# Kernel optimization log

Hardware: AMD Instinct MI355X
Metric: run time of the kernel (lower is better)

The kernel has to match this reference:

```python
import jax, jax.numpy as jnp
import numpy as np

DIM = 512
HEADS = 8
DIM_HEAD = DIM // 8          # 64
INNER = HEADS * DIM_HEAD     # 512
M_LANDMARKS = DIM // 2       # 256
PINV_ITERS = 6
RES_KERNEL = 33
LN_EPS = 1e-5


def setup_inputs() -> dict:
    key = jax.random.key(0)
    ks = jax.random.split(key, 7)
    b, n = 8, 4096
    x = jax.random.normal(ks[0], (b, n, DIM), dtype=jnp.float32)
    gamma = jnp.ones((DIM,), jnp.float32)
    beta = jnp.zeros((DIM,), jnp.float32)
    w_qkv = jax.random.normal(ks[1], (DIM, 3 * INNER), jnp.float32) * 0.02
    w_out = jax.random.normal(ks[2], (INNER, DIM), jnp.float32) * 0.02
    b_out = jnp.zeros((DIM,), jnp.float32)
    # depthwise Conv2d(heads, heads, (33,1), groups=heads): torch weight [H,1,33,1]
    res_kernel = jax.random.normal(ks[3], (HEADS, 1, RES_KERNEL, 1), jnp.float32) * 0.05
    return {"x": x, "gamma": gamma, "beta": beta, "w_qkv": w_qkv,
            "w_out": w_out, "b_out": b_out, "res_kernel": res_kernel}


def _moore_penrose_pinv(a, iters=PINV_ITERS):
    # a: [b, h, m, m]
    abs_a = jnp.abs(a)
    col = abs_a.sum(axis=-1).max()   # global max, as in torch.max(col)
    row = abs_a.sum(axis=-2).max()
    z = jnp.swapaxes(a, -1, -2) / (col * row)
    I = jnp.eye(a.shape[-1], dtype=a.dtype)
    for _ in range(iters):
        az = a @ z
        z = 0.25 * z @ (13. * I - az @ (15. * I - az @ (7. * I - az)))
    return z


def _nystrom_attention(xn, w_qkv, res_kernel, w_out, b_out):
    b, n, _ = xn.shape
    h, dh, m = HEADS, DIM_HEAD, M_LANDMARKS
    scale = dh ** -0.5
    qkv = xn @ w_qkv                               # [b, n, 3*inner]
    q, k, v = jnp.split(qkv, 3, axis=-1)
    def to_heads(t):
        return t.reshape(b, n, h, dh).transpose(0, 2, 1, 3)  # [b,h,n,dh]
    q, k, v = to_heads(q), to_heads(k), to_heads(v)
    q = q * scale

    l = n // m  # n chosen as multiple of m -> no padding branch
    # landmark pooling: '(m l) d -> m d' mean
    q_l = q.reshape(b, h, m, l, dh).mean(axis=3)   # [b,h,m,dh]
    k_l = k.reshape(b, h, m, l, dh).mean(axis=3)

    sim1 = jnp.einsum('bhid,bhjd->bhij', q, k_l)    # [b,h,n,m]
    sim2 = jnp.einsum('bhid,bhjd->bhij', q_l, k_l)  # [b,h,m,m]
    sim3 = jnp.einsum('bhid,bhjd->bhij', q_l, k)    # [b,h,m,n]

    attn1 = jax.nn.softmax(sim1, axis=-1)
    attn2 = jax.nn.softmax(sim2, axis=-1)
    attn3 = jax.nn.softmax(sim3, axis=-1)

    attn2_inv = _moore_penrose_pinv(attn2)
    out = (attn1 @ attn2_inv) @ (attn3 @ v)         # [b,h,n,dh]

    # residual depthwise conv over sequence dim (kernel 33x1, groups=heads)
    pad = RES_KERNEL // 2
    out = out + jax.lax.conv_general_dilated(
        v, res_kernel, window_strides=(1, 1),
        padding=((pad, pad), (0, 0)),
        dimension_numbers=('NCHW', 'OIHW', 'NCHW'),
        feature_group_count=HEADS)

    out = out.transpose(0, 2, 1, 3).reshape(b, n, h * dh)  # [b,n,inner]
    return out @ w_out + b_out  # dropout omitted (eval mode)


def reference(x, gamma, beta, w_qkv, w_out, b_out, res_kernel):
    mu = x.mean(axis=-1, keepdims=True)
    var = x.var(axis=-1, keepdims=True)
    xn = (x - mu) * jax.lax.rsqrt(var + LN_EPS) * gamma + beta
    return x + _nystrom_attention(xn, w_qkv, res_kernel, w_out, b_out)
```

## Files before the change

### kernel.cpp

```cpp
#include <hip/hip_runtime.h>

#define SEQ 4096
#define DMODEL 512
#define NH 8
#define DH 64
#define MLM 256
#define NBH 64
#define NROWS 32768

typedef unsigned short bf16_t;
typedef __attribute__((ext_vector_type(8))) short bf16x8;
typedef __attribute__((ext_vector_type(4))) float f32x4;

__device__ __forceinline__ float bf2f(unsigned short u) {
  return __uint_as_float(((unsigned)u) << 16);
}
__device__ __forceinline__ unsigned short f2bf(float f) {
  unsigned u = __float_as_uint(f);
  u += 0x7fffu + ((u >> 16) & 1u);
  return (unsigned short)(u >> 16);
}
__device__ __forceinline__ void unp8(const bf16_t* p, float* d) {
  uint4 u = *(const uint4*)p;
  d[0] = __uint_as_float(u.x << 16); d[1] = __uint_as_float(u.x & 0xffff0000u);
  d[2] = __uint_as_float(u.y << 16); d[3] = __uint_as_float(u.y & 0xffff0000u);
  d[4] = __uint_as_float(u.z << 16); d[5] = __uint_as_float(u.z & 0xffff0000u);
  d[6] = __uint_as_float(u.w << 16); d[7] = __uint_as_float(u.w & 0xffff0000u);
}

__device__ __forceinline__ void gll(const void* g, void* l) {
  __builtin_amdgcn_global_load_lds(
      (const __attribute__((address_space(1))) unsigned int*)g,
      (__attribute__((address_space(3))) unsigned int*)l, 16, 0, 0);
}

__global__ __launch_bounds__(64) void ln_kernel(const float* __restrict__ x,
    const float* __restrict__ gamma, const float* __restrict__ beta,
    bf16_t* __restrict__ xn) {
  int row = blockIdx.x;
  const float4* xr = (const float4*)(x + (size_t)row * DMODEL);
  int t = threadIdx.x;
  float4 a = xr[t], b = xr[t + 64];
  float s  = a.x + a.y + a.z + a.w + b.x + b.y + b.z + b.w;
  float ss = a.x*a.x + a.y*a.y + a.z*a.z + a.w*a.w
           + b.x*b.x + b.y*b.y + b.z*b.z + b.w*b.w;
#pragma unroll
  for (int off = 32; off > 0; off >>= 1) {
    s  += __shfl_xor(s, off);
    ss += __shfl_xor(ss, off);
  }
  float mean = s * (1.0f / DMODEL);
  float var  = ss * (1.0f / DMODEL) - mean * mean;
  float rstd = rsqrtf(var + 1e-5f);
  const float4* g4 = (const float4*)gamma;
  const float4* be4 = (const float4*)beta;
  ushort4* o = (ushort4*)(xn + (size_t)row * DMODEL);
  float4 g = g4[t], bb = be4[t];
  ushort4 r;
  r.x = f2bf((a.x - mean) * rstd * g.x + bb.x);
  r.y = f2bf((a.y - mean) * rstd * g.y + bb.y);
  r.z = f2bf((a.z - mean) * rstd * g.z + bb.z);
  r.w = f2bf((a.w - mean) * rstd * g.w + bb.w);
  o[t] = r;
  g = g4[t + 64]; bb = be4[t + 64];
  r.x = f2bf((b.x - mean) * rstd * g.x + bb.x);
  r.y = f2bf((b.y - mean) * rstd * g.y + bb.y);
  r.z = f2bf((b.z - mean) * rstd * g.z + bb.z);
  r.w = f2bf((b.w - mean) * rstd * g.w + bb.w);
  o[t + 64] = r;
}

__global__ __launch_bounds__(256) void convT2(const float* __restrict__ wqkv,
    const float* __restrict__ wout, bf16_t* __restrict__ wqkvT,
    bf16_t* __restrict__ woutT, unsigned* __restrict__ scal) {
  if (blockIdx.x == 0 && threadIdx.x < 2) scal[threadIdx.x] = 0u;
  size_t idx = (size_t)blockIdx.x * 256 + threadIdx.x;
  if (idx < 786432) {
    int n = (int)(idx / 512), k = (int)(idx % 512);
    wqkvT[idx] = f2bf(wqkv[(size_t)k * 1536 + n]);
  } else {
    size_t j = idx - 786432;
    int n = (int)(j / 512), k = (int)(j % 512);
    woutT[j] = f2bf(wout[(size_t)k * 512 + n]);
  }
}

#define MFMA_GEMM_BODY(APTR, BTPTR, KDIM) \
  __shared__ short As[128][32]; \
  __shared__ short Bs[128][32]; \
  int tid = threadIdx.x; \
  int lane = tid & 63; \
  int wv = tid >> 6; \
  int wm = (wv & 1) << 6, wn = (wv >> 1) << 6; \
  int l15 = lane & 15, l16 = lane >> 4; \
  f32x4 acc[4][4]; \
  _Pragma("unroll") for (int fm = 0; fm < 4; ++fm) \
    _Pragma("unroll") for (int fn = 0; fn < 4; ++fn) \
      acc[fm][fn] = (f32x4){0.f, 0.f, 0.f, 0.f}; \
  int ar0 = tid >> 2, ac0 = (tid & 3) << 3; \
  const bf16_t* Ab  = (APTR) + (size_t)(m0 + ar0) * (KDIM) + ac0; \
  const bf16_t* Ab1 = (APTR) + (size_t)(m0 + ar0 + 64) * (KDIM) + ac0; \
  const bf16_t* Bb  = (BTPTR) + (size_t)(n0 + ar0) * (KDIM) + ac0; \
  const bf16_t* Bb1 = (BTPTR) + (size_t)(n0 + ar0 + 64) * (KDIM) + ac0; \
  short* AsW  = &As[(wv << 4)][0]; \
  short* AsW1 = &As[64 + (wv << 4)][0]; \
  short* BsW  = &Bs[(wv << 4)][0]; \
  short* BsW1 = &Bs[64 + (wv << 4)][0]; \
  for (int k0 = 0; k0 < (KDIM); k0 += 32) { \
    gll(Ab + k0, AsW);  gll(Ab1 + k0, AsW1); \
    gll(Bb + k0, BsW);  gll(Bb1 + k0, BsW1); \
    __syncthreads(); \
    bf16x8 af[4], bfr[4]; \
    _Pragma("unroll") for (int f = 0; f < 4; ++f) { \
      af[f]  = *(const bf16x8*)&As[wm + f * 16 + l15][l16 * 8]; \
      bfr[f] = *(const bf16x8*)&Bs[wn + f * 16 + l15][l16 * 8]; \
    } \
    _Pragma("unroll") for (int fm = 0; fm < 4; ++fm) \
      _Pragma("unroll") for (int fn = 0; fn < 4; ++fn) \
        acc[fm][fn] = __builtin_amdgcn_mfma_f32_16x16x32_bf16(af[fm], bfr[fn], acc[fm][fn], 0, 0, 0); \
    __syncthreads(); \
  }

#define BMM256_BODY(APTR, BTPTR) \
  __shared__ short As[32][264]; \
  __shared__ short Bs[32][264]; \
  int tid = threadIdx.x; \
  int lane = tid & 63; \
  int wv = tid >> 6; \
  int wm = (wv & 1) << 4, wn = (wv >> 1) << 4; \
  int l15 = lane & 15, l16 = lane >> 4; \
  int ar0 = tid >> 3, ac0 = (tid & 7) << 2; \
  const bf16_t* Ab = (APTR) + (size_t)(m0 + ar0) * 256 + ac0; \
  const bf16_t* Bb = (BTPTR) + (size_t)(n0 + ar0) * 256 + ac0; \
  uint2 ga[8], gb[8]; \
  _Pragma("unroll") for (int u = 0; u < 8; ++u) { \
    ga[u] = *(const uint2*)(Ab + u * 32); gb[u] = *(const uint2*)(Bb + u * 32); } \
  _Pragma("unroll") for (int u = 0; u < 8; ++u) { \
    *(uint2*)&As[ar0][ac0 + u * 32] = ga[u]; *(uint2*)&Bs[ar0][ac0 + u * 32] = gb[u]; } \
  __syncthreads(); \
  f32x4 acc = (f32x4){0.f, 0.f, 0.f, 0.f}; \
  _Pragma("unroll") for (int u = 0; u < 8; ++u) { \
    bf16x8 af = *(const bf16x8*)&As[wm + l15][u * 32 + l16 * 8]; \
    bf16x8 bf = *(const bf16x8*)&Bs[wn + l15][u * 32 + l16 * 8]; \
    acc = __builtin_amdgcn_mfma_f32_16x16x32_bf16(af, bf, acc, 0, 0, 0); }

__global__ __launch_bounds__(512) void gemm_qkv_256(const bf16_t* __restrict__ A,
    const bf16_t* __restrict__ BT, bf16_t* __restrict__ q, bf16_t* __restrict__ k,
    bf16_t* __restrict__ vT, bf16_t* __restrict__ qlb, bf16_t* __restrict__ klb) {
  int bid = blockIdx.x;
  int orig = (bid & 7) * 96 + (bid >> 3);
  int n0 = (orig % 6) << 8;
  int m0 = (orig / 6) << 8;
  __shared__ short As[4][8192];
  __shared__ short Bs[4][8192];
  int tid = threadIdx.x;
  int lane = tid & 63;
  int wid = tid >> 6;
  int wr = wid >> 2, wc = wid & 3;
  int l15 = lane & 15, l16 = lane >> 4;
  int sl = (l16 ^ (l15 & 3)) << 3;
  int gr  = lane >> 2;
  int gcs = ((lane & 3) ^ ((lane >> 2) & 3)) << 3;
  f32x4 acc[8][4];
#pragma unroll
  for (int fm = 0; fm < 8; ++fm)
#pragma unroll
    for (int fn = 0; fn < 4; ++fn) acc[fm][fn] = (f32x4){0.f, 0.f, 0.f, 0.f};

#define STAGE(kt, s) { \
    _Pragma("unroll") for (int u = 0; u < 2; ++u) { \
      int r0 = (wid << 5) + (u << 4); \
      gll(A  + (size_t)(m0 + r0 + gr) * 512 + (kt) * 32 + gcs, &As[s][r0 << 5]); \
      gll(BT + (size_t)(n0 + r0 + gr) * 512 + (kt) * 32 + gcs, &Bs[s][r0 << 5]); \
    } }

  STAGE(0, 0) STAGE(1, 1) STAGE(2, 2)
  for (int t = 0; t < 16; ++t) {
    int s = t & 3;
    if (t < 14)       asm volatile("s_waitcnt vmcnt(8)" ::: "memory");
    else if (t == 14) asm volatile("s_waitcnt vmcnt(4)" ::: "memory");
    else              asm volatile("s_waitcnt vmcnt(0)" ::: "memory");
    __builtin_amdgcn_s_barrier();
    if (t + 3 < 16) STAGE(t + 3, ((t + 3) & 3))
    bf16x8 a[8], b[4];
#pragma unroll
    for (int fm = 0; fm < 8; ++fm)
      a[fm] = *(const bf16x8*)&As[s][(((wr << 7) + (fm << 4) + l15) << 5) + sl];
#pragma unroll
    for (int fn = 0; fn < 4; ++fn)
      b[fn] = *(const bf16x8*)&Bs[s][(((wc << 6) + (fn << 4) + l15) << 5) + sl];
    asm volatile("s_waitcnt lgkmcnt(0)" ::: "memory");
    __builtin_amdgcn_sched_barrier(0);
    __builtin_amdgcn_s_setprio(1);
#pragma unroll
    for (int fm = 0; fm < 8; ++fm)
#pragma unroll
      for (int fn = 0; fn < 4; ++fn)
        acc[fm][fn] = __builtin_amdgcn_mfma_f32_16x16x32_bf16(a[fm], b[fn], acc[fm][fn], 0, 0, 0);
    __builtin_amdgcn_s_setprio(0);
  }
#undef STAGE
#pragma unroll
  for (int fm = 0; fm < 8; ++fm) {
    int row0 = m0 + (wr << 7) + (fm << 4) + (l16 << 2);
    int bat = row0 >> 12;
    int nn0 = row0 & 4095;
    int lm  = nn0 >> 4;
#pragma unroll
    for (int fn = 0; fn < 4; ++fn) {
      int col = n0 + (wc << 6) + (fn << 4) + l15;
      int which = col >> 9;
      int hd = (col >> 6) & 7;
      int d  = col & 63;
      if (which == 2) {
        ushort4 pk;
        pk.x = f2bf(acc[fm][fn][0]); pk.y = f2bf(acc[fm][fn][1]);
        pk.z = f2bf(acc[fm][fn][2]); pk.w = f2bf(acc[fm][fn][3]);
        *(ushort4*)(vT + ((size_t)(bat * NH + hd) * DH + d) * SEQ + nn0) = pk;
      } else {
        bf16_t* dst = (which == 0) ? q : k;
        float scale = (which == 0) ? 0.125f : 1.f;
#pragma unroll
        for (int rg = 0; rg < 4; ++rg)
          dst[(((size_t)(bat * NH + hd)) * SEQ + nn0 + rg) * DH + d] = f2bf(acc[fm][fn][rg] * scale);
        float s = acc[fm][fn][0] + acc[fm][fn][1] + acc[fm][fn][2] + acc[fm][fn][3];
        s += __shfl_xor(s, 16);
        s += __shfl_xor(s, 32);
        if (l16 == 0) {
          bf16_t* pdst = (which == 0) ? qlb : klb;
          pdst[((size_t)(bat * NH + hd) * MLM + lm) * DH + d] = f2bf(s * scale * 0.0625f);
        }
      }
    }
  }
}

__global__ __launch_bounds__(256) void gemm_out_mfma(const bf16_t* __restrict__ A,
    const bf16_t* __restrict__ BT, const float* __restrict__ bias,
    const float* __restrict__ x, float* __restrict__ y) {
  int bid = blockIdx.x;
  int orig = (bid & 7) * 128 + (bid >> 3);
  int n0 = (orig & 3) << 7;
  int m0 = (orig >> 2) << 7;
  MFMA_GEMM_BODY(A, BT, 512)
#pragma unroll
  for (int fm = 0; fm < 4; ++fm) {
#pragma unroll
    for (int fn = 0; fn < 4; ++fn) {
      int col = n0 + wn + fn * 16 + l15;
      float bv = bias[col];
#pragma unroll
      for (int rg = 0; rg < 4; ++rg) {
        int row = m0 + wm + fm * 16 + l16 * 4 + rg;
        y[(size_t)row * DMODEL + col] = x[(size_t)row * DMODEL + col] + acc[fm][fn][rg] + bv;
      }
    }
  }
}

__global__ __launch_bounds__(256) void bmm_mfma32(const bf16_t* __restrict__ Ag,
    const bf16_t* __restrict__ BTg, bf16_t* __restrict__ Cb,
    bf16_t* __restrict__ CTb, float* __restrict__ Cf,
    int K, float alpha, float eA, float diagc, int flags) {
  int bid = blockIdx.x;
  int orig = (bid & 7) * 512 + (bid >> 3);
  int bh = orig >> 6;
  int tile = orig & 63;
  int n0 = (tile & 7) << 5;
  int m0 = (tile >> 3) << 5;
  const bf16_t* A  = Ag + (size_t)bh * 256 * K;
  const bf16_t* BT = BTg + (size_t)bh * 256 * K;
  __shared__ short As[32][264];
  __shared__ short Bs[32][264];
  int tid = threadIdx.x;
  int lane = tid & 63;
  int wv = tid >> 6;
  int wm = (wv & 1) << 4, wn = (wv >> 1) << 4;
  int l15 = lane & 15, l16 = lane >> 4;
  int ar0 = tid >> 3, ac0 = (tid & 7) << 2;
  const bf16_t* Ab = A + (size_t)(m0 + ar0) * K + ac0;
  const bf16_t* Bb = BT + (size_t)(n0 + ar0) * K + ac0;
  int nch = K >> 5;
  uint2 ga[8], gb[8];
#pragma unroll 8
  for (int u = 0; u < 8; ++u)
    if (u < nch) { ga[u] = *(const uint2*)(Ab + u * 32); gb[u] = *(const uint2*)(Bb + u * 32); }
#pragma unroll 8
  for (int u = 0; u < 8; ++u)
    if (u < nch) { *(uint2*)&As[ar0][ac0 + u * 32] = ga[u]; *(uint2*)&Bs[ar0][ac0 + u * 32] = gb[u]; }
  __syncthreads();
  f32x4 acc = (f32x4){0.f, 0.f, 0.f, 0.f};
#pragma unroll 8
  for (int u = 0; u < 8; ++u)
    if (u < nch) {
      bf16x8 af = *(const bf16x8*)&As[wm + l15][u * 32 + l16 * 8];
      bf16x8 bf = *(const bf16x8*)&Bs[wn + l15][u * 32 + l16 * 8];
      acc = __builtin_amdgcn_mfma_f32_16x16x32_bf16(af, bf, acc, 0, 0, 0);
    }
  size_t cbase = (size_t)bh * 65536;
  int row0 = m0 + wm + l16 * 4;
  int col = n0 + wn + l15;
  float v4[4];
#pragma unroll
  for (int rg = 0; rg < 4; ++rg) {
    float val = alpha * acc[rg];
    if (eA != 0.f) val += eA * bf2f(A[(size_t)(row0 + rg) * K + col]);
    if (row0 + rg == col) val += diagc;
    v4[rg] = val;
  }
  if (flags & 1) {
#pragma unroll
    for (int rg = 0; rg < 4; ++rg)
      Cb[cbase + (size_t)(row0 + rg) * 256 + col] = f2bf(v4[rg]);
  }
  if (flags & 2) {
    ushort4 pk;
    pk.x = f2bf(v4[0]); pk.y = f2bf(v4[1]);
    pk.z = f2bf(v4[2]); pk.w = f2bf(v4[3]);
    *(ushort4*)(CTb + cbase + (size_t)col * 256 + row0) = pk;
  }
  if (flags & 4) {
#pragma unroll
    for (int rg = 0; rg < 4; ++rg)
      Cf[cbase + (size_t)(row0 + rg) * 256 + col] = v4[rg];
  }
}

__global__ __launch_bounds__(256) void pinv_WU(const bf16_t* __restrict__ Yc,
    const bf16_t* __restrict__ YTc, const bf16_t* __restrict__ zc,
    const bf16_t* __restrict__ t1Tp, bf16_t* __restrict__ Wb,
    bf16_t* __restrict__ UT, bf16_t* __restrict__ zo) {
  int bid = blockIdx.x;
  int cpx = gridDim.x >> 3;
  int orig = (bid & 7) * cpx + (bid >> 3);
  int zt = orig >> 12;
  int o = orig & 4095;
  int bh = o >> 6;
  int tile = o & 63;
  int n0 = (tile & 7) << 5;
  int m0 = (tile >> 3) << 5;
  const bf16_t* A  = (zt ? zc : Yc) + ((size_t)bh << 16);
  const bf16_t* BT = (zt ? t1Tp : YTc) + ((size_t)bh << 16);
  BMM256_BODY(A, BT)
  size_t cbase = (size_t)bh << 16;
  int row0 = m0 + wm + l16 * 4;
  int col = n0 + wn + l15;
  if (zt) {
#pragma unroll
    for (int rg = 0; rg < 4; ++rg)
      zo[cbase + (size_t)(row0 + rg) * 256 + col] = f2bf(0.25f * acc[rg]);
  } else {
    ushort4 pk;
    unsigned short uv[4];
#pragma unroll
    for (int rg = 0; rg < 4; ++rg) {
      float w = acc[rg];
      float y = bf2f(Yc[cbase + (size_t)(row0 + rg) * 256 + col]);
      Wb[cbase + (size_t)(row0 + rg) * 256 + col] = f2bf(w);
      uv[rg] = f2bf(7.f * y - w);
    }
    pk.x = uv[0]; pk.y = uv[1]; pk.z = uv[2]; pk.w = uv[3];
    *(ushort4*)(UT + cbase + (size_t)col * 256 + row0) = pk;
  }
}

__global__ __launch_bounds__(256) void pinv_E(const bf16_t* __restrict__ Yc,
    const bf16_t* __restrict__ Wb, const bf16_t* __restrict__ UT,
    bf16_t* __restrict__ Yo, bf16_t* __restrict__ YTo,
    bf16_t* __restrict__ t1T) {
  int bid = blockIdx.x;
  int orig = (bid & 7) * 1024 + (bid >> 3);
  int task = orig >> 12;
  int o = orig & 4095;
  int bh = o >> 6;
  int tile = o & 63;
  int n0 = (tile & 7) << 5;
  int m0 = (tile >> 3) << 5;
  const bf16_t* A  = (task ? Yc : Wb) + ((size_t)bh << 16);
  const bf16_t* BT = UT + ((size_t)bh << 16);
  BMM256_BODY(A, BT)
  size_t cbase = (size_t)bh << 16;
  int row0 = m0 + wm + l16 * 4;
  int col = n0 + wn + l15;
  if (task == 0) {
    ushort4 pk;
    unsigned short yv[4];
#pragma unroll
    for (int rg = 0; rg < 4; ++rg) {
      size_t idx = cbase + (size_t)(row0 + rg) * 256 + col;
      float y = bf2f(Yc[idx]);
      float w = bf2f(Wb[idx]);
      float v = 0.25f * acc[rg] + 3.25f * y - 3.75f * w;
      yv[rg] = f2bf(v);
      Yo[idx] = yv[rg];
    }
    pk.x = yv[0]; pk.y = yv[1]; pk.z = yv[2]; pk.w = yv[3];
    *(ushort4*)(YTo + cbase + (size_t)col * 256 + row0) = pk;
  } else {
    ushort4 pk;
    unsigned short tv[4];
#pragma unroll
    for (int rg = 0; rg < 4; ++rg) {
      float y = bf2f(Yc[cbase + (size_t)(row0 + rg) * 256 + col]);
      float v = acc[rg] - 15.f * y;
      if (row0 + rg == col) v += 13.f;
      tv[rg] = f2bf(v);
    }
    pk.x = tv[0]; pk.y = tv[1]; pk.z = tv[2]; pk.w = tv[3];
    *(ushort4*)(t1T + cbase + (size_t)col * 256 + row0) = pk;
  }
}

__global__ __launch_bounds__(256) void softmax256(const float* __restrict__ af,
    bf16_t* __restrict__ ab) {
  const float* ar = af + (size_t)blockIdx.x * MLM;
  int t = threadIdx.x;
  float v = ar[t];
  __shared__ float redm[4], reds[4];
  float m = v;
#pragma unroll
  for (int off = 32; off > 0; off >>= 1) m = fmaxf(m, __shfl_xor(m, off));
  if ((t & 63) == 0) redm[t >> 6] = m;
  __syncthreads();
  m = fmaxf(fmaxf(redm[0], redm[1]), fmaxf(redm[2], redm[3]));
  float p = __expf(v - m);
  float s = p;
#pragma unroll
  for (int off = 32; off > 0; off >>= 1) s += __shfl_xor(s, off);
  if ((t & 63) == 0) reds[t >> 6] = s;
  __syncthreads();
  s = reds[0] + reds[1] + reds[2] + reds[3];
  ab[(size_t)blockIdx.x * MLM + t] = f2bf(p / s);
}

__global__ __launch_bounds__(256) void colrow_max(const bf16_t* __restrict__ a,
    unsigned* __restrict__ scal) {
  int bh = blockIdx.x;
  int task = blockIdx.y;
  const bf16_t* ab = a + (size_t)bh * MLM * MLM;
  int t = threadIdx.x;
  float s = 0.f;
  if (task == 0) {
    const bf16_t* rp = ab + (size_t)t * MLM;
    for (int j = 0; j < MLM; j += 8) {
      float d[8];
      unp8(rp + j, d);
      s += d[0]; s += d[1]; s += d[2]; s += d[3];
      s += d[4]; s += d[5]; s += d[6]; s += d[7];
    }
  } else {
    for (int i = 0; i < MLM; ++i) s += bf2f(ab[(size_t)i * MLM + t]);
  }
  __shared__ float red[4];
  float m = s;
#pragma unroll
  for (int off = 32; off > 0; off >>= 1) m = fmaxf(m, __shfl_xor(m, off));
  if ((t & 63) == 0) red[t >> 6] = m;
  __syncthreads();
  if (t == 0) {
    m = fmaxf(fmaxf(red[0], red[1]), fmaxf(red[2], red[3]));
    atomicMax(scal + task, __float_as_uint(m));
  }
}

__global__ __launch_bounds__(64) void attn3v_mfma(const bf16_t* __restrict__ qlb,
    const bf16_t* __restrict__ kg, const bf16_t* __restrict__ vT,
    float* __restrict__ pacc, float* __restrict__ pm, float* __restrict__ ps) {
  int bid = blockIdx.x;
  int orig = (bid & 7) * 512 + (bid >> 3);
  int m0 = (orig & 7) << 5;
  int cz = (orig >> 3) & 7;
  int bh = orig >> 6;
  int lane = threadIdx.x;
  int l15 = lane & 15, l16 = lane >> 4;
  __shared__ short plds[32][136];
  const bf16_t* qbase = qlb + (size_t)bh * MLM * DH;
  const bf16_t* kbase = kg + (size_t)bh * SEQ * DH;
  const bf16_t* vbase = vT + (size_t)bh * DH * SEQ;
  bf16x8 af[2][2];
#pragma unroll
  for (int mt = 0; mt < 2; ++mt)
#pragma unroll
    for (int ks = 0; ks < 2; ++ks)
      af[mt][ks] = *(const bf16x8*)(qbase + (size_t)(m0 + mt * 16 + l15) * DH + ks * 32 + l16 * 8);
  float m_run[2][4], s_run[2][4];
  f32x4 o[2][4];
#pragma unroll
  for (int mt = 0; mt < 2; ++mt) {
#pragma unroll
    for (int rg = 0; rg < 4; ++rg) { m_run[mt][rg] = -1e30f; s_run[mt][rg] = 0.f; }
#pragma unroll
    for (int n2 = 0; n2 < 4; ++n2) o[mt][n2] = (f32x4){0.f, 0.f, 0.f, 0.f};
  }
  int kbeg = cz << 9;
  for (int kt = kbeg; kt < kbeg + 512; kt += 128) {
    f32x4 sacc[2][8];
#pragma unroll
    for (int mt = 0; mt < 2; ++mt)
#pragma unroll
      for (int nt = 0; nt < 8; ++nt) sacc[mt][nt] = (f32x4){0.f, 0.f, 0.f, 0.f};
#pragma unroll
    for (int nt = 0; nt < 8; ++nt) {
      const bf16_t* kr = kbase + (size_t)(kt + nt * 16 + l15) * DH + l16 * 8;
      bf16x8 b0 = *(const bf16x8*)kr;
      bf16x8 b1 = *(const bf16x8*)(kr + 32);
      sacc[0][nt] = __builtin_amdgcn_mfma_f32_16x16x32_bf16(af[0][0], b0, sacc[0][nt], 0, 0, 0);
      sacc[0][nt] = __builtin_amdgcn_mfma_f32_16x16x32_bf16(af[0][1], b1, sacc[0][nt], 0, 0, 0);
      sacc[1][nt] = __builtin_amdgcn_mfma_f32_16x16x32_bf16(af[1][0], b0, sacc[1][nt], 0, 0, 0);
      sacc[1][nt] = __builtin_amdgcn_mfma_f32_16x16x32_bf16(af[1][1], b1, sacc[1][nt], 0, 0, 0);
    }
#pragma unroll
    for (int mt = 0; mt < 2; ++mt)
#pragma unroll
      for (int rg = 0; rg < 4; ++rg) {
        float mx = sacc[mt][0][rg];
#pragma unroll
        for (int nt = 1; nt < 8; ++nt) mx = fmaxf(mx, sacc[mt][nt][rg]);
        mx = fmaxf(mx, __shfl_xor(mx, 1));
        mx = fmaxf(mx, __shfl_xor(mx, 2));
        mx = fmaxf(mx, __shfl_xor(mx, 4));
        mx = fmaxf(mx, __shfl_xor(mx, 8));
        float mnew = fmaxf(m_run[mt][rg], mx);
        float corr = __expf(m_run[mt][rg] - mnew);
        float s = 0.f;
#pragma unroll
        for (int nt = 0; nt < 8; ++nt) {
          float p = __expf(sacc[mt][nt][rg] - mnew);
          sacc[mt][nt][rg] = p;
          s += p;
        }
        s += __shfl_xor(s, 1); s += __shfl_xor(s, 2);
        s += __shfl_xor(s, 4); s += __shfl_xor(s, 8);
        s_run[mt][rg] = s_run[mt][rg] * corr + s;
        m_run[mt][rg] = mnew;
#pragma unroll
        for (int n2 = 0; n2 < 4; ++n2) o[mt][n2][rg] *= corr;
      }
#pragma unroll
    for (int mt = 0; mt < 2; ++mt)
#pragma unroll
      for (int nt = 0; nt < 8; ++nt)
#pragma unroll
        for (int rg = 0; rg < 4; ++rg)
          plds[mt * 16 + l16 * 4 + rg][nt * 16 + l15] = (short)f2bf(sacc[mt][nt][rg]);
#pragma unroll
    for (int ks2 = 0; ks2 < 4; ++ks2) {
      bf16x8 pa0 = *(const bf16x8*)&plds[l15][ks2 * 32 + l16 * 8];
      bf16x8 pa1 = *(const bf16x8*)&plds[16 + l15][ks2 * 32 + l16 * 8];
#pragma unroll
      for (int n2 = 0; n2 < 4; ++n2) {
        bf16x8 vb8 = *(const bf16x8*)(vbase + (size_t)(n2 * 16 + l15) * SEQ + kt + ks2 * 32 + l16 * 8);
        o[0][n2] = __builtin_amdgcn_mfma_f32_16x16x32_bf16(pa0, vb8, o[0][n2], 0, 0, 0);
        o[1][n2] = __builtin_amdgcn_mfma_f32_16x16x32_bf16(pa1, vb8, o[1][n2], 0, 0, 0);
      }
    }
  }
  size_t pidx0 = (size_t)(bh * 8 + cz) * MLM + m0;
#pragma unroll
  for (int mt = 0; mt < 2; ++mt)
#pragma unroll
    for (int n2 = 0; n2 < 4; ++n2)
#pragma unroll
      for (int rg = 0; rg < 4; ++rg) {
        int row = mt * 16 + l16 * 4 + rg;
        pacc[(pidx0 + row) * 64 + n2 * 16 + l15] = o[mt][n2][rg];
      }
  if (l15 == 0) {
#pragma unroll
    for (int mt = 0; mt < 2; ++mt)
#pragma unroll
      for (int rg = 0; rg < 4; ++rg) {
        pm[pidx0 + mt * 16 + l16 * 4 + rg] = m_run[mt][rg];
        ps[pidx0 + mt * 16 + l16 * 4 + rg] = s_run[mt][rg];
      }
  }
}

__global__ __launch_bounds__(256) void comb_zinit(const float* __restrict__ pacc,
    const float* __restrict__ pm, const float* __restrict__ ps,
    bf16_t* __restrict__ a3vb, const bf16_t* __restrict__ ab,
    bf16_t* __restrict__ z0, bf16_t* __restrict__ z0T,
    const unsigned* __restrict__ scal) {
  if (blockIdx.x < 4096) {
    int gw = blockIdx.x * 4 + (threadIdx.x >> 6);
    int lane = threadIdx.x & 63;
    int bh = gw >> 8, row = gw & 255;
    float ms[8];
    float M = -1e30f;
#pragma unroll
    for (int cc = 0; cc < 8; ++cc) {
      ms[cc] = pm[(size_t)(bh * 8 + cc) * MLM + row];
      M = fmaxf(M, ms[cc]);
    }
    float S = 0.f, val = 0.f;
#pragma unroll
    for (int cc = 0; cc < 8; ++cc) {
      size_t pidx = (size_t)(bh * 8 + cc) * MLM + row;
      float w = __expf(ms[cc] - M);
      S += w * ps[pidx];
      val += w * pacc[pidx * 64 + lane];
    }
    a3vb[(size_t)gw * 64 + lane] = f2bf(val / S);
  } else {
    size_t idx = (size_t)(blockIdx.x - 4096) * 256 + threadIdx.x;
    float denom = __uint_as_float(scal[0]) * __uint_as_float(scal[1]);
    size_t bh = idx >> 16;
    int i = (int)((idx >> 8) & 255);
    int j = (int)(idx & 255);
    bf16_t r = f2bf(bf2f(ab[idx]) / denom);
    z0T[idx] = r;
    z0[(bh << 16) + ((size_t)j << 8) + i] = r;
  }
}

__global__ __launch_bounds__(256) void wm_kernel(const bf16_t* __restrict__ zb,
    const bf16_t* __restrict__ a3vb, bf16_t* __restrict__ wmT) {
  int bh = blockIdx.y;
  int m0 = blockIdx.x << 6;
  __shared__ bf16_t a3s[MLM * DH];
  int t = threadIdx.x;
  const bf16_t* asrc = a3vb + (size_t)bh * MLM * DH;
#pragma unroll
  for (int i = 0; i < 8; ++i)
    *(bf16x8*)(a3s + ((size_t)t + 256 * i) * 8) =
        *(const bf16x8*)(asrc + ((size_t)t + 256 * i) * 8);
  __syncthreads();
  int row = m0 + (t >> 2);
  int c0 = (t & 3) * 16;
  const bf16_t* zrow = zb + (size_t)bh * 65536 + (size_t)row * 256;
  float acc16[16] = {};
  for (int k0 = 0; k0 < 256; k0 += 8) {
    float a8[8];
    unp8(zrow + k0, a8);
#pragma unroll
    for (int j = 0; j < 8; ++j) {
      float av[16];
      unp8(a3s + (k0 + j) * 64 + c0, av);
      unp8(a3s + (k0 + j) * 64 + c0 + 8, av + 8);
#pragma unroll
      for (int e = 0; e < 16; ++e) acc16[e] += a8[j] * av[e];
    }
  }
  bf16_t* wd = wmT + (size_t)bh * DH * MLM;
#pragma unroll
  for (int e = 0; e < 16; ++e)
    wd[(size_t)(c0 + e) * MLM + row] = f2bf(acc16[e]);
}

__global__ __launch_bounds__(64) void attn1_mfma(const bf16_t* __restrict__ qg,
    const bf16_t* __restrict__ klb, const bf16_t* __restrict__ wmT,
    bf16_t* __restrict__ om) {
  int bh = blockIdx.y, bat = bh >> 3, head = bh & 7;
  int m0 = blockIdx.x << 5;
  int lane = threadIdx.x;
  int l15 = lane & 15, l16 = lane >> 4;
  __shared__ short plds[32][264];
  const bf16_t* qbase = qg + (size_t)bh * SEQ * DH;
  const bf16_t* kbase = klb + (size_t)bh * MLM * DH;
  bf16x8 af[2][2];
#pragma unroll
  for (int mt = 0; mt < 2; ++mt)
#pragma unroll
    for (int ks = 0; ks < 2; ++ks)
      af[mt][ks] = *(const bf16x8*)(qbase + (size_t)(m0 + mt * 16 + l15) * DH + ks * 32 + l16 * 8);
  f32x4 acc[2][16];
#pragma unroll
  for (int mt = 0; mt < 2; ++mt)
#pragma unroll
    for (int nt = 0; nt < 16; ++nt) acc[mt][nt] = (f32x4){0.f, 0.f, 0.f, 0.f};
#pragma unroll
  for (int nt = 0; nt < 16; ++nt) {
    bf16x8 b0 = *(const bf16x8*)(kbase + (size_t)(nt * 16 + l15) * DH + l16 * 8);
    bf16x8 b1 = *(const bf16x8*)(kbase + (size_t)(nt * 16 + l15) * DH + 32 + l16 * 8);
    acc[0][nt] = __builtin_amdgcn_mfma_f32_16x16x32_bf16(af[0][0], b0, acc[0][nt], 0, 0, 0);
    acc[0][nt] = __builtin_amdgcn_mfma_f32_16x16x32_bf16(af[0][1], b1, acc[0][nt], 0, 0, 0);
    acc[1][nt] = __builtin_amdgcn_mfma_f32_16x16x32_bf16(af[1][0], b0, acc[1][nt], 0, 0, 0);
    acc[1][nt] = __builtin_amdgcn_mfma_f32_16x16x32_bf16(af[1][1], b1, acc[1][nt], 0, 0, 0);
  }
  float inv[2][4];
#pragma unroll
  for (int mt = 0; mt < 2; ++mt)
#pragma unroll
    for (int rg = 0; rg < 4; ++rg) {
      float mx = acc[mt][0][rg];
#pragma unroll
      for (int nt = 1; nt < 16; ++nt) mx = fmaxf(mx, acc[mt][nt][rg]);
      mx = fmaxf(mx, __shfl_xor(mx, 1));
      mx = fmaxf(mx, __shfl_xor(mx, 2));
      mx = fmaxf(mx, __shfl_xor(mx, 4));
      mx = fmaxf(mx, __shfl_xor(mx, 8));
      float s = 0.f;
#pragma unroll
      for (int nt = 0; nt < 16; ++nt) {
        float p = __expf(acc[mt][nt][rg] - mx);
        acc[mt][nt][rg] = p;
        s += p;
      }
      s += __shfl_xor(s, 1); s += __shfl_xor(s, 2);
      s += __shfl_xor(s, 4); s += __shfl_xor(s, 8);
      inv[mt][rg] = 1.f / s;
    }
#pragma unroll
  for (int mt = 0; mt < 2; ++mt)
#pragma unroll
    for (int nt = 0; nt < 16; ++nt)
#pragma unroll
      for (int rg = 0; rg < 4; ++rg)
        plds[mt * 16 + l16 * 4 + rg][nt * 16 + l15] = (short)f2bf(acc[mt][nt][rg]);
  const bf16_t* wbase = wmT + (size_t)bh * DH * MLM;
  f32x4 o[2][4];
#pragma unroll
  for (int mt = 0; mt < 2; ++mt)
#pragma unroll
    for (int n2 = 0; n2 < 4; ++n2) o[mt][n2] = (f32x4){0.f, 0.f, 0.f, 0.f};
#pragma unroll
  for (int ks = 0; ks < 8; ++ks) {
    bf16x8 pa0 = *(const bf16x8*)&plds[l15][ks * 32 + l16 * 8];
    bf16x8 pa1 = *(const bf16x8*)&plds[16 + l15][ks * 32 + l16 * 8];
#pragma unroll
    for (int n2 = 0; n2 < 4; ++n2) {
      bf16x8 wb = *(const bf16x8*)(wbase + (size_t)(n2 * 16 + l15) * MLM + ks * 32 + l16 * 8);
      o[0][n2] = __builtin_amdgcn_mfma_f32_16x16x32_bf16(pa0, wb, o[0][n2], 0, 0, 0);
      o[1][n2] = __builtin_amdgcn_mfma_f32_16x16x32_bf16(pa1, wb, o[1][n2], 0, 0, 0);
    }
  }
#pragma unroll
  for (int mt = 0; mt < 2; ++mt)
#pragma unroll
    for (int n2 = 0; n2 < 4; ++n2)
#pragma unroll
      for (int rg = 0; rg < 4; ++rg) {
        int n = m0 + mt * 16 + l16 * 4 + rg;
        int d = n2 * 16 + l15;
        om[((size_t)(bat * SEQ + n)) * DMODEL + head * DH + d] =
            f2bf(o[mt][n2][rg] * inv[mt][rg]);
      }
}

__global__ __launch_bounds__(256) void conv_add(const bf16_t* __restrict__ vT,
    const float* __restrict__ rk, bf16_t* __restrict__ om) {
  int bh = blockIdx.y, bat = bh >> 3, head = bh & 7;
  int n0 = blockIdx.x << 5;
  __shared__ bf16_t vs[64 * 64];
  int t = threadIdx.x;
  int d = t & 63;
  int nq = (t >> 6) << 4;
  const bf16_t* vrow = vT + ((size_t)bh * DH + d) * SEQ;
#pragma unroll
  for (int h = 0; h < 2; ++h) {
    int nb = n0 - 16 + nq + h * 8;
    unsigned short tmp[8];
    if (nb >= 0 && nb + 8 <= SEQ) {
      bf16x8 val = *(const bf16x8*)(vrow + nb);
#pragma unroll
      for (int e = 0; e < 8; ++e) tmp[e] = ((unsigned short*)&val)[e];
    } else {
#pragma unroll
      for (int e = 0; e < 8; ++e) {
        int n = nb + e;
        tmp[e] = (n >= 0 && n < SEQ) ? vrow[n] : (unsigned short)0;
      }
    }
#pragma unroll
    for (int e = 0; e < 8; ++e) vs[(nq + h * 8 + e) * 64 + d] = tmp[e];
  }
  __syncthreads();
  float w[33];
#pragma unroll
  for (int i = 0; i < 33; ++i) w[i] = rk[head * 33 + i];
  int r0 = (t >> 6) << 3;
  float out[8] = {0.f, 0.f, 0.f, 0.f, 0.f, 0.f, 0.f, 0.f};
#pragma unroll
  for (int j = 0; j < 40; ++j) {
    float vv = bf2f(vs[(r0 + j) * 64 + d]);
    int ilo = j - 32; if (ilo < 0) ilo = 0;
    int ihi = j; if (ihi > 7) ihi = 7;
    for (int i = ilo; i <= ihi; ++i) out[i] += w[j - i] * vv;
  }
#pragma unroll
  for (int i = 0; i < 8; ++i) {
    int n = n0 + r0 + i;
    size_t idx = ((size_t)(bat * SEQ + n)) * DMODEL + head * DH + d;
    om[idx] = f2bf(bf2f(om[idx]) + out[i]);
  }
}

extern "C" void kernel_launch(void* const* d_in, const int* in_sizes, int n_in,
                              void* d_out, int out_size, void* d_ws, size_t ws_size,
                              hipStream_t stream) {
  const float* x     = (const float*)d_in[0];
  const float* gamma = (const float*)d_in[1];
  const float* beta  = (const float*)d_in[2];
  const float* w_qkv = (const float*)d_in[3];
  const float* w_out = (const float*)d_in[4];
  const float* b_out = (const float*)d_in[5];
  const float* rk    = (const float*)d_in[6];
  float* y  = (float*)d_out;

  bf16_t* xnb  = (bf16_t*)d_ws;
  bf16_t* qb   = xnb + 16777216;
  bf16_t* kb   = qb + 16777216;
  bf16_t* vTb  = kb + 16777216;
  bf16_t* wqkvT = vTb + 16777216;
  bf16_t* woutT = wqkvT + 786432;
  bf16_t* qlb  = woutT + 262144;
  bf16_t* klb  = qlb + 1048576;
  bf16_t* a2b  = klb + 1048576;
  bf16_t* zA   = a2b + 4194304;
  bf16_t* z0T  = zA + 4194304;
  bf16_t* zB   = z0T + 4194304;
  bf16_t* Ya   = zB + 4194304;
  bf16_t* Yb   = z0T;
  bf16_t* a3vb = Ya + 4194304;
  bf16_t* wmT  = a3vb + 1048576;
  float*  SR   = (float*)(wmT + 1048576);
  float*  a2f  = SR;
  float*  pacc = SR;
  bf16_t* YTa  = (bf16_t*)SR;
  bf16_t* YTb  = YTa + 4194304;
  bf16_t* Wb   = YTa + 8388608;
  bf16_t* t1T  = YTa + 12582912;
  bf16_t* UT   = xnb;
  float*  pm   = SR + 8388608;
  float*  ps   = pm + 131072;
  unsigned* scal = (unsigned*)(ps + 131072);
  size_t need = (size_t)93323264 * 2 + (size_t)(8388608 + 262144) * 4 + 64;
  if (ws_size < need) return;

  ln_kernel<<<NROWS, 64, 0, stream>>>(x, gamma, beta, xnb);
  convT2<<<4096, 256, 0, stream>>>(w_qkv, w_out, wqkvT, woutT, scal);

  gemm_qkv_256<<<768, 512, 0, stream>>>(xnb, wqkvT, qb, kb, vTb, qlb, klb);

  bmm_mfma32<<<4096, 256, 0, stream>>>(qlb, klb, nullptr, nullptr, a2f,
      64, 1.f, 0.f, 0.f, 4);
  softmax256<<<NBH * MLM, 256, 0, stream>>>(a2f, a2b);
  colrow_max<<<dim3(NBH, 2), 256, 0, stream>>>(a2b, scal);

  attn3v_mfma<<<4096, 64, 0, stream>>>(qlb, kb, vTb, pacc, pm, ps);
  comb_zinit<<<20480, 256, 0, stream>>>(pacc, pm, ps, a3vb, a2b, zA, z0T, scal);

  bmm_mfma32<<<4096, 256, 0, stream>>>(a2b, z0T, Ya, YTa, nullptr,
      256, 1.f, 0.f, 0.f, 3);

  bf16_t* zc = zA;  bf16_t* zo = zB;
  bf16_t* Yc = Ya;  bf16_t* YTc = YTa;
  bf16_t* Yo = Yb;  bf16_t* YTo = YTb;
  for (int it = 0; it < 6; ++it) {
    if (it == 0) {
      pinv_WU<<<4096, 256, 0, stream>>>(Yc, YTc, nullptr, nullptr, Wb, UT, nullptr);
    } else {
      pinv_WU<<<8192, 256, 0, stream>>>(Yc, YTc, zc, t1T, Wb, UT, zo);
      bf16_t* tp = zc; zc = zo; zo = tp;
    }
    pinv_E<<<8192, 256, 0, stream>>>(Yc, Wb, UT, Yo, YTo, t1T);
    bf16_t* tp;
    tp = Yc; Yc = Yo; Yo = tp;
    tp = YTc; YTc = YTo; YTo = tp;
  }
  bmm_mfma32<<<4096, 256, 0, stream>>>(zc, t1T, zo, nullptr, nullptr,
      256, 0.25f, 0.f, 0.f, 1);
  { bf16_t* tp = zc; zc = zo; zo = tp; }

  wm_kernel<<<dim3(4, NBH), 256, 0, stream>>>(zc, a3vb, wmT);

  bf16_t* om = xnb;
  attn1_mfma<<<dim3(SEQ / 32, NBH), 64, 0, stream>>>(qb, klb, wmT, om);
  conv_add<<<dim3(SEQ / 32, NBH), 256, 0, stream>>>(vTb, rk, om);

  gemm_out_mfma<<<1024, 256, 0, stream>>>(om, woutT, b_out, x, y);
}
```

Measured before the change: 760.3 us.

## Use 64x64 tiles for pinv GEMMs and fuse residual conv into attn1

The Newton-Schulz pinv kernels move from 32x32 output tiles (one MFMA accumulator per wave) to 64x64 tiles where each wave computes a 2x2 block of MFMA fragments. This cuts the block count fourfold and reuses each loaded A/B fragment across more MFMAs, at the cost of a larger LDS footprint per block. Separately, the depthwise 33-tap residual conv is folded into attn1_mfma's epilogue. It reuses the attention kernel's shared memory and removes a separate launch and its read-modify-write of the bf16 output. The fused conv runs on a single 64-lane wave per block, so that work is now spread over fewer threads.

```diff
diff --git a/kernel.cpp b/kernel.cpp
--- a/kernel.cpp
+++ b/kernel.cpp
@@ -143,6 +143,37 @@
     bf16x8 af = *(const bf16x8*)&As[wm + l15][u * 32 + l16 * 8]; \
     bf16x8 bf = *(const bf16x8*)&Bs[wn + l15][u * 32 + l16 * 8]; \
     acc = __builtin_amdgcn_mfma_f32_16x16x32_bf16(af, bf, acc, 0, 0, 0); }
+
+#define BMM64_BODY(APTR, BTPTR) \
+  __shared__ short As[64][264]; \
+  __shared__ short Bs[64][264]; \
+  int tid = threadIdx.x; \
+  int lane = tid & 63; \
+  int wv = tid >> 6; \
+  int wr = wv >> 1, wc = wv & 1; \
+  int l15 = lane & 15, l16 = lane >> 4; \
+  int ar0 = tid >> 2, ac0 = (tid & 3) << 6; \
+  const bf16_t* Ab = (APTR) + (size_t)(m0 + ar0) * 256 + ac0; \
+  const bf16_t* Bb = (BTPTR) + (size_t)(n0 + ar0) * 256 + ac0; \
+  uint4 ga[8], gb[8]; \
+  _Pragma("unroll") for (int u = 0; u < 8; ++u) { \
+    ga[u] = *(const uint4*)(Ab + u * 8); gb[u] = *(const uint4*)(Bb + u * 8); } \
+  _Pragma("unroll") for (int u = 0; u < 8; ++u) { \
+    *(uint4*)&As[ar0][ac0 + u * 8] = ga[u]; *(uint4*)&Bs[ar0][ac0 + u * 8] = gb[u]; } \
+  __syncthreads(); \
+  f32x4 acc[2][2]; \
+  _Pragma("unroll") for (int fm = 0; fm < 2; ++fm) \
+    _Pragma("unroll") for (int fn = 0; fn < 2; ++fn) \
+      acc[fm][fn] = (f32x4){0.f, 0.f, 0.f, 0.f}; \
+  _Pragma("unroll") for (int u = 0; u < 8; ++u) { \
+    bf16x8 a0 = *(const bf16x8*)&As[(wr << 5) + l15][u * 32 + l16 * 8]; \
+    bf16x8 a1 = *(const bf16x8*)&As[(wr << 5) + 16 + l15][u * 32 + l16 * 8]; \
+    bf16x8 b0 = *(const bf16x8*)&Bs[(wc << 5) + l15][u * 32 + l16 * 8]; \
+    bf16x8 b1 = *(const bf16x8*)&Bs[(wc << 5) + 16 + l15][u * 32 + l16 * 8]; \
+    acc[0][0] = __builtin_amdgcn_mfma_f32_16x16x32_bf16(a0, b0, acc[0][0], 0, 0, 0); \
+    acc[0][1] = __builtin_amdgcn_mfma_f32_16x16x32_bf16(a0, b1, acc[0][1], 0, 0, 0); \
+    acc[1][0] = __builtin_amdgcn_mfma_f32_16x16x32_bf16(a1, b0, acc[1][0], 0, 0, 0); \
+    acc[1][1] = __builtin_amdgcn_mfma_f32_16x16x32_bf16(a1, b1, acc[1][1], 0, 0, 0); }
 
 __global__ __launch_bounds__(512) void gemm_qkv_256(const bf16_t* __restrict__ A,
     const bf16_t* __restrict__ BT, bf16_t* __restrict__ q, bf16_t* __restrict__ k,
@@ -326,89 +357,106 @@
   }
 }
 
-__global__ __launch_bounds__(256) void pinv_WU(const bf16_t* __restrict__ Yc,
+__global__ __launch_bounds__(256) void pinv_WU64(const bf16_t* __restrict__ Yc,
     const bf16_t* __restrict__ YTc, const bf16_t* __restrict__ zc,
     const bf16_t* __restrict__ t1Tp, bf16_t* __restrict__ Wb,
     bf16_t* __restrict__ UT, bf16_t* __restrict__ zo) {
   int bid = blockIdx.x;
   int cpx = gridDim.x >> 3;
   int orig = (bid & 7) * cpx + (bid >> 3);
-  int zt = orig >> 12;
-  int o = orig & 4095;
-  int bh = o >> 6;
-  int tile = o & 63;
-  int n0 = (tile & 7) << 5;
-  int m0 = (tile >> 3) << 5;
+  int zt = orig >> 10;
+  int o = orig & 1023;
+  int bh = o >> 4;
+  int tile = o & 15;
+  int n0 = (tile & 3) << 6;
+  int m0 = (tile >> 2) << 6;
   const bf16_t* A  = (zt ? zc : Yc) + ((size_t)bh << 16);
   const bf16_t* BT = (zt ? t1Tp : YTc) + ((size_t)bh << 16);
-  BMM256_BODY(A, BT)
+  BMM64_BODY(A, BT)
   size_t cbase = (size_t)bh << 16;
-  int row0 = m0 + wm + l16 * 4;
-  int col = n0 + wn + l15;
   if (zt) {
 #pragma unroll
-    for (int rg = 0; rg < 4; ++rg)
-      zo[cbase + (size_t)(row0 + rg) * 256 + col] = f2bf(0.25f * acc[rg]);
+    for (int fm = 0; fm < 2; ++fm)
+#pragma unroll
+      for (int fn = 0; fn < 2; ++fn) {
+        int row0 = m0 + (wr << 5) + fm * 16 + (l16 << 2);
+        int col  = n0 + (wc << 5) + fn * 16 + l15;
+#pragma unroll
+        for (int rg = 0; rg < 4; ++rg)
+          zo[cbase + (size_t)(row0 + rg) * 256 + col] = f2bf(0.25f * acc[fm][fn][rg]);
+      }
   } else {
-    ushort4 pk;
-    unsigned short uv[4];
-#pragma unroll
-    for (int rg = 0; rg < 4; ++rg) {
-      float w = acc[rg];
-      float y = bf2f(Yc[cbase + (size_t)(row0 + rg) * 256 + col]);
-      Wb[cbase + (size_t)(row0 + rg) * 256 + col] = f2bf(w);
-      uv[rg] = f2bf(7.f * y - w);
-    }
-    pk.x = uv[0]; pk.y = uv[1]; pk.z = uv[2]; pk.w = uv[3];
-    *(ushort4*)(UT + cbase + (size_t)col * 256 + row0) = pk;
-  }
-}
-
-__global__ __launch_bounds__(256) void pinv_E(const bf16_t* __restrict__ Yc,
+#pragma unroll
+    for (int fm = 0; fm < 2; ++fm)
+#pragma unroll
+      for (int fn = 0; fn < 2; ++fn) {
+        int row0 = m0 + (wr << 5) + fm * 16 + (l16 << 2);
+        int col  = n0 + (wc << 5) + fn * 16 + l15;
+        ushort4 pk;
+        unsigned short uv[4];
+#pragma unroll
+        for (int rg = 0; rg < 4; ++rg) {
+          float w = acc[fm][fn][rg];
+          float y = bf2f(Yc[cbase + (size_t)(row0 + rg) * 256 + col]);
+          Wb[cbase + (size_t)(row0 + rg) * 256 + col] = f2bf(w);
+          uv[rg] = f2bf(7.f * y - w);
+        }
+        pk.x = uv[0]; pk.y = uv[1]; pk.z = uv[2]; pk.w = uv[3];
+        *(ushort4*)(UT + cbase + (size_t)col * 256 + row0) = pk;
+      }
+  }
+}
+
+__global__ __launch_bounds__(256) void pinv_E64(const bf16_t* __restrict__ Yc,
     const bf16_t* __restrict__ Wb, const bf16_t* __restrict__ UT,
     bf16_t* __restrict__ Yo, bf16_t* __restrict__ YTo,
     bf16_t* __restrict__ t1T) {
   int bid = blockIdx.x;
-  int orig = (bid & 7) * 1024 + (bid >> 3);
-  int task = orig >> 12;
-  int o = orig & 4095;
-  int bh = o >> 6;
-  int tile = o & 63;
-  int n0 = (tile & 7) << 5;
-  int m0 = (tile >> 3) << 5;
+  int orig = (bid & 7) * 256 + (bid >> 3);
+  int task = orig >> 10;
+  int o = orig & 1023;
+  int bh = o >> 4;
+  int tile = o & 15;
+  int n0 = (tile & 3) << 6;
+  int m0 = (tile >> 2) << 6;
   const bf16_t* A  = (task ? Yc : Wb) + ((size_t)bh << 16);
   const bf16_t* BT = UT + ((size_t)bh << 16);
-  BMM256_BODY(A, BT)
+  BMM64_BODY(A, BT)
   size_t cbase = (size_t)bh << 16;
-  int row0 = m0 + wm + l16 * 4;
-  int col = n0 + wn + l15;
-  if (task == 0) {
-    ushort4 pk;
-    unsigned short yv[4];
-#pragma unroll
-    for (int rg = 0; rg < 4; ++rg) {
-      size_t idx = cbase + (size_t)(row0 + rg) * 256 + col;
-      float y = bf2f(Yc[idx]);
-      float w = bf2f(Wb[idx]);
-      float v = 0.25f * acc[rg] + 3.25f * y - 3.75f * w;
-      yv[rg] = f2bf(v);
-      Yo[idx] = yv[rg];
-    }
-    pk.x = yv[0]; pk.y = yv[1]; pk.z = yv[2]; pk.w = yv[3];
-    *(ushort4*)(YTo + cbase + (size_t)col * 256 + row0) = pk;
-  } else {
-    ushort4 pk;
-    unsigned short tv[4];
-#pragma unroll
-    for (int rg = 0; rg < 4; ++rg) {
-      float y = bf2f(Yc[cbase + (size_t)(row0 + rg) * 256 + col]);
-      float v = acc[rg] - 15.f * y;
-      if (row0 + rg == col) v += 13.f;
-      tv[rg] = f2bf(v);
-    }
-    pk.x = tv[0]; pk.y = tv[1]; pk.z = tv[2]; pk.w = tv[3];
-    *(ushort4*)(t1T + cbase + (size_t)col * 256 + row0) = pk;
-  }
+#pragma unroll
+  for (int fm = 0; fm < 2; ++fm)
+#pragma unroll
+    for (int fn = 0; fn < 2; ++fn) {
+      int row0 = m0 + (wr << 5) + fm * 16 + (l16 << 2);
+      int col  = n0 + (wc << 5) + fn * 16 + l15;
+      if (task == 0) {
+        ushort4 pk;
+        unsigned short yv[4];
+#pragma unroll
+        for (int rg = 0; rg < 4; ++rg) {
+          size_t idx = cbase + (size_t)(row0 + rg) * 256 + col;
+          float y = bf2f(Yc[idx]);
+          float w = bf2f(Wb[idx]);
+          float v = 0.25f * acc[fm][fn][rg] + 3.25f * y - 3.75f * w;
+          yv[rg] = f2bf(v);
+          Yo[idx] = yv[rg];
+        }
+        pk.x = yv[0]; pk.y = yv[1]; pk.z = yv[2]; pk.w = yv[3];
+        *(ushort4*)(YTo + cbase + (size_t)col * 256 + row0) = pk;
+      } else {
+        ushort4 pk;
+        unsigned short tv[4];
+#pragma unroll
+        for (int rg = 0; rg < 4; ++rg) {
+          float y = bf2f(Yc[cbase + (size_t)(row0 + rg) * 256 + col]);
+          float v = acc[fm][fn][rg] - 15.f * y;
+          if (row0 + rg == col) v += 13.f;
+          tv[rg] = f2bf(v);
+        }
+        pk.x = tv[0]; pk.y = tv[1]; pk.z = tv[2]; pk.w = tv[3];
+        *(ushort4*)(t1T + cbase + (size_t)col * 256 + row0) = pk;
+      }
+    }
 }
 
 __global__ __launch_bounds__(256) void softmax256(const float* __restrict__ af,
@@ -649,6 +697,7 @@
 
 __global__ __launch_bounds__(64) void attn1_mfma(const bf16_t* __restrict__ qg,
     const bf16_t* __restrict__ klb, const bf16_t* __restrict__ wmT,
+    const bf16_t* __restrict__ vT, const float* __restrict__ rk,
     bf16_t* __restrict__ om) {
   int bh = blockIdx.y, bat = bh >> 3, head = bh & 7;
   int m0 = blockIdx.x << 5;
@@ -724,65 +773,56 @@
       o[1][n2] = __builtin_amdgcn_mfma_f32_16x16x32_bf16(pa1, wb, o[1][n2], 0, 0, 0);
     }
   }
-#pragma unroll
-  for (int mt = 0; mt < 2; ++mt)
-#pragma unroll
-    for (int n2 = 0; n2 < 4; ++n2)
-#pragma unroll
-      for (int rg = 0; rg < 4; ++rg) {
-        int n = m0 + mt * 16 + l16 * 4 + rg;
-        int d = n2 * 16 + l15;
-        om[((size_t)(bat * SEQ + n)) * DMODEL + head * DH + d] =
-            f2bf(o[mt][n2][rg] * inv[mt][rg]);
-      }
-}
-
-__global__ __launch_bounds__(256) void conv_add(const bf16_t* __restrict__ vT,
-    const float* __restrict__ rk, bf16_t* __restrict__ om) {
-  int bh = blockIdx.y, bat = bh >> 3, head = bh & 7;
-  int n0 = blockIdx.x << 5;
-  __shared__ bf16_t vs[64 * 64];
-  int t = threadIdx.x;
-  int d = t & 63;
-  int nq = (t >> 6) << 4;
-  const bf16_t* vrow = vT + ((size_t)bh * DH + d) * SEQ;
-#pragma unroll
-  for (int h = 0; h < 2; ++h) {
-    int nb = n0 - 16 + nq + h * 8;
-    unsigned short tmp[8];
+  __syncthreads();
+  bf16_t* vs = (bf16_t*)&plds[0][0];
+  float*  cv = (float*)((char*)&plds[0][0] + 8192);
+  const bf16_t* vrow = vT + ((size_t)bh * DH + lane) * SEQ;
+#pragma unroll
+  for (int h = 0; h < 8; ++h) {
+    int nb = m0 - 16 + h * 8;
     if (nb >= 0 && nb + 8 <= SEQ) {
       bf16x8 val = *(const bf16x8*)(vrow + nb);
 #pragma unroll
-      for (int e = 0; e < 8; ++e) tmp[e] = ((unsigned short*)&val)[e];
+      for (int e = 0; e < 8; ++e) vs[(h * 8 + e) * 64 + lane] = ((unsigned short*)&val)[e];
     } else {
 #pragma unroll
       for (int e = 0; e < 8; ++e) {
         int n = nb + e;
-        tmp[e] = (n >= 0 && n < SEQ) ? vrow[n] : (unsigned short)0;
-      }
-    }
-#pragma unroll
-    for (int e = 0; e < 8; ++e) vs[(nq + h * 8 + e) * 64 + d] = tmp[e];
+        vs[(h * 8 + e) * 64 + lane] = (n >= 0 && n < SEQ) ? vrow[n] : (unsigned short)0;
+      }
+    }
   }
   __syncthreads();
   float w[33];
 #pragma unroll
   for (int i = 0; i < 33; ++i) w[i] = rk[head * 33 + i];
-  int r0 = (t >> 6) << 3;
-  float out[8] = {0.f, 0.f, 0.f, 0.f, 0.f, 0.f, 0.f, 0.f};
-#pragma unroll
-  for (int j = 0; j < 40; ++j) {
-    float vv = bf2f(vs[(r0 + j) * 64 + d]);
-    int ilo = j - 32; if (ilo < 0) ilo = 0;
-    int ihi = j; if (ihi > 7) ihi = 7;
-    for (int i = ilo; i <= ihi; ++i) out[i] += w[j - i] * vv;
-  }
-#pragma unroll
-  for (int i = 0; i < 8; ++i) {
-    int n = n0 + r0 + i;
-    size_t idx = ((size_t)(bat * SEQ + n)) * DMODEL + head * DH + d;
-    om[idx] = f2bf(bf2f(om[idx]) + out[i]);
-  }
+#pragma unroll
+  for (int g = 0; g < 4; ++g) {
+    int r0 = g * 8;
+    float out[8] = {0.f, 0.f, 0.f, 0.f, 0.f, 0.f, 0.f, 0.f};
+#pragma unroll
+    for (int j = 0; j < 40; ++j) {
+      float vv = bf2f(vs[(r0 + j) * 64 + lane]);
+      int ilo = j - 32; if (ilo < 0) ilo = 0;
+      int ihi = j; if (ihi > 7) ihi = 7;
+      for (int i = ilo; i <= ihi; ++i) out[i] += w[j - i] * vv;
+    }
+#pragma unroll
+    for (int i = 0; i < 8; ++i) cv[(r0 + i) * 64 + lane] = out[i];
+  }
+  __syncthreads();
+#pragma unroll
+  for (int mt = 0; mt < 2; ++mt)
+#pragma unroll
+    for (int n2 = 0; n2 < 4; ++n2)
+#pragma unroll
+      for (int rg = 0; rg < 4; ++rg) {
+        int nr = mt * 16 + l16 * 4 + rg;
+        int d = n2 * 16 + l15;
+        float base = bf2f(f2bf(o[mt][n2][rg] * inv[mt][rg]));
+        om[((size_t)(bat * SEQ + m0 + nr)) * DMODEL + head * DH + d] =
+            f2bf(base + cv[nr * 64 + d]);
+      }
 }
 
 extern "C" void kernel_launch(void* const* d_in, const int* in_sizes, int n_in,
@@ -848,12 +888,12 @@
   bf16_t* Yo = Yb;  bf16_t* YTo = YTb;
   for (int it = 0; it < 6; ++it) {
     if (it == 0) {
-      pinv_WU<<<4096, 256, 0, stream>>>(Yc, YTc, nullptr, nullptr, Wb, UT, nullptr);
+      pinv_WU64<<<1024, 256, 0, stream>>>(Yc, YTc, nullptr, nullptr, Wb, UT, nullptr);
     } else {
-      pinv_WU<<<8192, 256, 0, stream>>>(Yc, YTc, zc, t1T, Wb, UT, zo);
+      pinv_WU64<<<2048, 256, 0, stream>>>(Yc, YTc, zc, t1T, Wb, UT, zo);
       bf16_t* tp = zc; zc = zo; zo = tp;
     }
-    pinv_E<<<8192, 256, 0, stream>>>(Yc, Wb, UT, Yo, YTo, t1T);
+    pinv_E64<<<2048, 256, 0, stream>>>(Yc, Wb, UT, Yo, YTo, t1T);
     bf16_t* tp;
     tp = Yc; Yc = Yo; Yo = tp;
     tp = YTc; YTc = YTo; YTo = tp;
@@ -865,8 +905,7 @@
   wm_kernel<<<dim3(4, NBH), 256, 0, stream>>>(zc, a3vb, wmT);
 
   bf16_t* om = xnb;
-  attn1_mfma<<<dim3(SEQ / 32, NBH), 64, 0, stream>>>(qb, klb, wmT, om);
-  conv_add<<<dim3(SEQ / 32, NBH), 256, 0, stream>>>(vTb, rk, om);
+  attn1_mfma<<<dim3(SEQ / 32, NBH), 64, 0, stream>>>(qb, klb, wmT, vTb, rk, om);
 
   gemm_out_mfma<<<1024, 256, 0, stream>>>(om, woutT, b_out, x, y);
 }
```

New measurement: 789.9 us. +3.9%, slower.
